# Performance work log

Measured on AMD Instinct MI355X. Metric: run time of the kernel, lower is better.

The kernel has to match this reference:

```python
import jax, jax.numpy as jnp
import numpy as np

B, L, D, H = 4, 2048, 1024, 16
DK = D // H  # 64


def setup_inputs() -> dict:
    key = jax.random.key(0)
    ks = jax.random.split(key, 5)
    x = jax.random.normal(ks[0], (B, L, D), dtype=jnp.float32)
    scale = 1.0 / np.sqrt(D)
    W_qkv = jax.random.normal(ks[1], (D, 3 * D), dtype=jnp.float32) * scale
    b_qkv = jnp.zeros((3 * D,), dtype=jnp.float32)
    W_out = jax.random.normal(ks[2], (D, D), dtype=jnp.float32) * scale
    b_out = jnp.zeros((D,), dtype=jnp.float32)
    return {"x": x, "W_qkv": W_qkv, "b_qkv": b_qkv, "W_out": W_out, "b_out": b_out}


def reference(x, W_qkv, b_qkv, W_out, b_out):
    Bx, Lx, Dx = x.shape
    qkv = x @ W_qkv + b_qkv                      # [B, L, 3D]
    q, k, v = jnp.split(qkv, 3, axis=-1)
    # [B, H, L, d_k]
    q = q.reshape(Bx, Lx, H, DK).transpose(0, 2, 1, 3)
    k = k.reshape(Bx, Lx, H, DK).transpose(0, 2, 1, 3)
    v = v.reshape(Bx, Lx, H, DK).transpose(0, 2, 1, 3)
    scores = jnp.einsum('bhqd,bhkd->bhqk', q, k) / np.sqrt(DK)
    causal = jnp.tril(jnp.ones((Lx, Lx), dtype=bool))
    scores = jnp.where(causal[None, None], scores, -jnp.inf)
    attn = jax.nn.softmax(scores, axis=-1)       # [B, H, L, L]
    out = jnp.einsum('bhqk,bhkd->bhqd', attn, v)
    out = out.transpose(0, 2, 1, 3).reshape(Bx, Lx, Dx)
    return out @ W_out + b_out
```

## Files before the change

kernel.cpp:

```cpp
#include <hip/hip_runtime.h>
#include <stdint.h>

#define B_ 4
#define L_ 2048
#define D_ 1024
#define H_ 16
#define DK_ 64

typedef __attribute__((ext_vector_type(8))) short bf16x8;
typedef __attribute__((ext_vector_type(4))) float f32x4;
typedef unsigned short bfu;

#define MFMA(a, b, c) __builtin_amdgcn_mfma_f32_16x16x32_bf16((a), (b), (c), 0, 0, 0)

__device__ __forceinline__ unsigned short f2bf(float f) {
  union { float f; unsigned int u; } v; v.f = f;
  unsigned int u = v.u;
  return (unsigned short)((u + 0x7fffu + ((u >> 16) & 1u)) >> 16);
}

__device__ __forceinline__ void gll16(const void* g, void* l) {
  __builtin_amdgcn_global_load_lds(
      (const __attribute__((address_space(1))) void*)g,
      (__attribute__((address_space(3))) void*)l, 16, 0, 0);
}


__global__ __launch_bounds__(256) void cast_x(const float* __restrict__ in,
                                              bfu* __restrict__ out, int n4) {
  int i = blockIdx.x * 256 + threadIdx.x;
  if (i >= n4) return;
  float4 v = ((const float4*)in)[i];
  ushort4 o;
  o.x = f2bf(v.x); o.y = f2bf(v.y); o.z = f2bf(v.z); o.w = f2bf(v.w);
  ((ushort4*)out)[i] = o;
}

__global__ void transpose_cast(const float* __restrict__ in, bfu* __restrict__ out,
                               int R, int C) {
  __shared__ float tile[32][33];
  int c0 = blockIdx.x * 32, r0 = blockIdx.y * 32;
  int tx = threadIdx.x, ty = threadIdx.y;
#pragma unroll
  for (int i = ty; i < 32; i += 8)
    tile[i][tx] = in[(size_t)(r0 + i) * C + c0 + tx];
  __syncthreads();
#pragma unroll
  for (int i = ty; i < 32; i += 8)
    out[(size_t)(c0 + i) * R + r0 + tx] = f2bf(tile[tx][i]);
}


template <int EPI>
__global__ __launch_bounds__(512, 2) void gemm8(
    const bfu* __restrict__ A, const bfu* __restrict__ Bt,
    const float* __restrict__ bias, bfu* __restrict__ Qg, bfu* __restrict__ Kg,
    bfu* __restrict__ Vtg, float* __restrict__ Out, int M, int N, int K) {
  __shared__ __align__(16) bfu LDSb[65536];
  const int tid = threadIdx.x;
  const int lane = tid & 63;
  const int w = tid >> 6;
  const int wm = w >> 2, wn = w & 3;
  const int l15 = lane & 15, l4 = lane >> 4;

  const int nwg = gridDim.x;
  const int cpx = nwg >> 3;
  const int bid = (int)blockIdx.x;
  const int swz = (bid & 7) * cpx + (bid >> 3);
  const int m0 = (swz & 31) * 256;
  const int n0 = (swz >> 5) * 256;

#define STAGE(t_, ev_)                                                        \
  {                                                                           \
    const int c_ = (t_) & 1;                                                  \
    bfu* lb_ = ((ev_) == 0 || (ev_) == 3) ? (LDSb + c_ * 16384)               \
                                          : (LDSb + 32768 + c_ * 16384);      \
    const bfu* gs_ = ((ev_) == 0 || (ev_) == 3) ? A : Bt;                     \
    const int g0_ = ((ev_) == 0 || (ev_) == 3) ? m0 : n0;                     \
    _Pragma("unroll") for (int j_ = 0; j_ < 2; ++j_) {                        \
      int idx_ = j_ * 512 + tid;                                              \
      int r7_ = idx_ >> 3;                                                    \
      int row_;                                                               \
      if ((ev_) == 0) row_ = r7_ + ((r7_ >> 6) << 6);                         \
      else if ((ev_) == 3) row_ = 64 + r7_ + ((r7_ >> 6) << 6);               \
      else if ((ev_) == 1) row_ = r7_ + ((r7_ >> 5) << 5);                    \
      else row_ = 32 + r7_ + ((r7_ >> 5) << 5);                               \
      int c16_ = (idx_ & 7) ^ (row_ & 7);                                     \
      gll16(gs_ + (size_t)(g0_ + row_) * K + (t_) * 64 + c16_ * 8,            \
            (char*)lb_ + row_ * 128 + (idx_ & 7) * 16);                       \
    }                                                                         \
  }

#define VMCNT(n_) asm volatile("s_waitcnt vmcnt(" #n_ ")" ::: "memory")
#define BARRIER() asm volatile("s_barrier" ::: "memory")

  f32x4 acc[8][4] = {};
  bf16x8 af[4][2], bfA[2][2], bfB[2][2];

  auto lda = [&](int c, int half) {
    const char* base = (const char*)(LDSb + c * 16384);
#pragma unroll
    for (int mi = 0; mi < 4; ++mi)
#pragma unroll
      for (int kk = 0; kk < 2; ++kk) {
        int row = wm * 128 + half * 64 + mi * 16 + l15;
        int ch = (kk * 4 + l4) ^ (row & 7);
        af[mi][kk] = *(const bf16x8*)(base + row * 128 + ch * 16);
      }
  };
  auto ldb = [&](int c, int half, bf16x8 (*dst)[2]) {
    const char* base = (const char*)(LDSb + 32768 + c * 16384);
#pragma unroll
    for (int ni = 0; ni < 2; ++ni)
#pragma unroll
      for (int kk = 0; kk < 2; ++kk) {
        int row = wn * 64 + half * 32 + ni * 16 + l15;
        int ch = (kk * 4 + l4) ^ (row & 7);
        dst[ni][kk] = *(const bf16x8*)(base + row * 128 + ch * 16);
      }
  };

#define MM(mo_, no_, bfX_)                                                    \
  __builtin_amdgcn_s_setprio(1);                                              \
  _Pragma("unroll") for (int mi_ = 0; mi_ < 4; ++mi_)                         \
  _Pragma("unroll") for (int ni_ = 0; ni_ < 2; ++ni_)                         \
  _Pragma("unroll") for (int kk_ = 0; kk_ < 2; ++kk_)                         \
    acc[(mo_) + mi_][(no_) + ni_] =                                           \
        MFMA(af[mi_][kk_], bfX_[ni_][kk_], acc[(mo_) + mi_][(no_) + ni_]);    \
  __builtin_amdgcn_s_setprio(0);

  STAGE(0, 0); STAGE(0, 1); STAGE(0, 2); STAGE(0, 3);
  VMCNT(4);
  BARRIER();

  const int NT = K >> 6;
  for (int t = 0; t < NT - 1; ++t) {
    const int c = t & 1, tn = t + 1;
    lda(c, 0); ldb(c, 0, bfA);
    STAGE(tn, 0);
    MM(0, 0, bfA);
    VMCNT(4); BARRIER();
    ldb(c, 1, bfB);
    STAGE(tn, 1);
    MM(0, 2, bfB);
    VMCNT(4); BARRIER();
    lda(c, 1);
    STAGE(tn, 2);
    MM(4, 2, bfB);
    BARRIER();
    STAGE(tn, 3);
    MM(4, 0, bfA);
    VMCNT(4); BARRIER();
  }
  {
    const int c = (NT - 1) & 1;
    lda(c, 0); ldb(c, 0, bfA);
    MM(0, 0, bfA);
    VMCNT(2); BARRIER();
    ldb(c, 1, bfB);
    MM(0, 2, bfB);
    VMCNT(0); BARRIER();
    lda(c, 1);
    MM(4, 2, bfB);
    MM(4, 0, bfA);
  }

  if (EPI == 1) {
#pragma unroll
    for (int ni = 0; ni < 4; ++ni) {
      int gn = n0 + wn * 64 + ni * 16 + l15;
      float bv = bias[gn];
#pragma unroll
      for (int mi = 0; mi < 8; ++mi)
#pragma unroll
        for (int rg = 0; rg < 4; ++rg) {
          int gm = m0 + wm * 128 + mi * 16 + l4 * 4 + rg;
          Out[(size_t)gm * N + gn] = acc[mi][ni][rg] + bv;
        }
    }
  } else {
    const int sec = n0 >> 10;
    if (sec < 2) {
      bfu* dst = (sec == 0) ? Qg : Kg;
      const float scale = (sec == 0) ? 0.18033688011112042f : 1.0f;
#pragma unroll
      for (int ni = 0; ni < 4; ++ni) {
        int gn = n0 + wn * 64 + ni * 16 + l15;
        int rem = gn & 1023;
        int hh = rem >> 6, dk = rem & 63;
        float bv = bias[gn];
#pragma unroll
        for (int mi = 0; mi < 8; ++mi)
#pragma unroll
          for (int rg = 0; rg < 4; ++rg) {
            int gm = m0 + wm * 128 + mi * 16 + l4 * 4 + rg;
            int bb = gm >> 11, ll = gm & 2047;
            dst[(((size_t)(bb * H_ + hh)) * L_ + ll) * DK_ + dk] =
                f2bf((acc[mi][ni][rg] + bv) * scale);
          }
      }
    } else {
      __syncthreads();
#pragma unroll
      for (int ni = 0; ni < 4; ++ni) {
        int n_local = wn * 64 + ni * 16 + l15;
        int gn = n0 + n_local;
        float bv = bias[gn];
        int swzn = (n_local & 7) << 4;
#pragma unroll
        for (int mi = 0; mi < 8; ++mi) {
          int m_base = wm * 128 + mi * 16 + l4 * 4;
          int k6 = m_base & 63;
          int p0 = (m_base & ~63) |
                   ((k6 & 32) | (((k6 >> 2) & 3) << 3) | (((k6 >> 4) & 1) << 2));
          float v0 = acc[mi][ni][0] + bv, v1 = acc[mi][ni][1] + bv;
          float v2 = acc[mi][ni][2] + bv, v3 = acc[mi][ni][3] + bv;
          uint32_t w01, w23;
          asm("v_cvt_pk_bf16_f32 %0, %1, %2" : "=v"(w01) : "v"(v0), "v"(v1));
          asm("v_cvt_pk_bf16_f32 %0, %1, %2" : "=v"(w23) : "v"(v2), "v"(v3));
          *(uint32_t*)((char*)LDSb + n_local * 512 + ((2 * p0) ^ swzn)) = w01;
          *(uint32_t*)((char*)LDSb + n_local * 512 + ((2 * p0 + 4) ^ swzn)) = w23;
        }
      }
      __syncthreads();
      int n = tid >> 1;
      int cb = (tid & 1) * 16;
      int gnn = n0 + n;
      int hh = (gnn >> 6) & 15, dk = gnn & 63;
      size_t rowbase =
          (((size_t)((m0 >> 11) * H_ + hh)) * DK_ + dk) * L_ + (m0 & 2047);
#pragma unroll
      for (int j = 0; j < 16; ++j) {
        int ch = cb + j;
        bf16x8 vv = *(const bf16x8*)((char*)LDSb + n * 512 +
                                     ((ch * 16) ^ ((n & 7) << 4)));
        *(bf16x8*)(Vtg + rowbase + ch * 8) = vv;
      }
    }
  }
#undef STAGE
#undef VMCNT
#undef BARRIER
#undef MM
}


__global__ __launch_bounds__(256, 4) void attn(const bfu* __restrict__ Qg,
                                               const bfu* __restrict__ Kg,
                                               const bfu* __restrict__ Vtg,
                                               bfu* __restrict__ Ao) {
  __shared__ __align__(16) bfu Ks[2 * 64 * 64];
  __shared__ __align__(16) bfu Vs[2 * 64 * 64];
  __shared__ __align__(16) bfu Qs[64 * 64];

  const int tid = threadIdx.x;
  const int lane = tid & 63;
  const int w = tid >> 6;
  const int l15 = lane & 15, l4 = lane >> 4;

  const int hid = blockIdx.x;
  const int xcd = hid & 7, slot = hid >> 3;
  const int bh = (xcd << 3) | (slot >> 4);
  const int xq = slot & 15;
  const int b = bh >> 4, h = bh & 15;

  for (int seg = 0; seg < 2; ++seg) {
    const int qb = (seg == 0) ? xq : 31 - xq;
    const int q0 = qb * 64;
    const int nt = qb + 1;

#pragma unroll
    for (int i = 0; i < 2; ++i) {
      int lb = i * 256 + tid;
      int r = lb >> 3, c16 = (lb & 7) ^ (r & 7);
      gll16(Qg + ((size_t)bh * L_ + q0 + r) * DK_ + c16 * 8, (char*)Qs + lb * 16);
      gll16(Kg + ((size_t)bh * L_ + r) * DK_ + c16 * 8, (char*)Ks + lb * 16);
      gll16(Vtg + ((size_t)bh * DK_ + r) * L_ + c16 * 8, (char*)Vs + lb * 16);
    }
    asm volatile("s_waitcnt vmcnt(0)" ::: "memory");
    asm volatile("s_barrier" ::: "memory");

    bf16x8 qf[2];
#pragma unroll
    for (int kk = 0; kk < 2; ++kk) {
      int r = w * 16 + l15;
      int c16 = (kk * 4 + l4) ^ (r & 7);
      qf[kk] = *(const bf16x8*)((const char*)Qs + r * 128 + c16 * 16);
    }

    f32x4 acco[4] = {};
    float m = -1e30f, l = 0.f;

    for (int t = 0; t < nt; ++t) {
      const int cur = t & 1;
      const char* Kc = (const char*)Ks + cur * 8192;
      const char* Vc = (const char*)Vs + cur * 8192;

      if (t + 1 < nt) {
        const int nb = (t + 1) & 1, nkv = (t + 1) * 64;
#pragma unroll
        for (int i = 0; i < 2; ++i) {
          int lb = i * 256 + tid;
          int r = lb >> 3, c16 = (lb & 7) ^ (r & 7);
          gll16(Kg + ((size_t)bh * L_ + nkv + r) * DK_ + c16 * 8,
                (char*)Ks + nb * 8192 + lb * 16);
          gll16(Vtg + ((size_t)bh * DK_ + r) * L_ + nkv + c16 * 8,
                (char*)Vs + nb * 8192 + lb * 16);
        }
        asm volatile("s_waitcnt vmcnt(4)" ::: "memory");
      } else {
        asm volatile("s_waitcnt vmcnt(0)" ::: "memory");
      }
      asm volatile("s_barrier" ::: "memory");

      f32x4 s[4] = {};
      __builtin_amdgcn_s_setprio(1);
#pragma unroll
      for (int kk = 0; kk < 2; ++kk)
#pragma unroll
        for (int ni = 0; ni < 4; ++ni) {
          int r = ni * 16 + l15;
          int c16 = (kk * 4 + l4) ^ (r & 7);
          bf16x8 kf = *(const bf16x8*)(Kc + r * 128 + c16 * 16);
          s[ni] = MFMA(kf, qf[kk], s[ni]);
        }
      __builtin_amdgcn_s_setprio(0);

      if (t == nt - 1) {
        int ql = w * 16 + l15;
#pragma unroll
        for (int ni = 0; ni < 4; ++ni) {
          int kvl = ni * 16 + l4 * 4;
#pragma unroll
          for (int rg = 0; rg < 4; ++rg)
            if (kvl + rg > ql) s[ni][rg] = -1e30f;
        }
      }

      float mx = fmaxf(fmaxf(fmaxf(s[0][0], s[0][1]), fmaxf(s[0][2], s[0][3])),
                       fmaxf(fmaxf(s[1][0], s[1][1]), fmaxf(s[1][2], s[1][3])));
      mx = fmaxf(mx, fmaxf(fmaxf(fmaxf(s[2][0], s[2][1]), fmaxf(s[2][2], s[2][3])),
                           fmaxf(fmaxf(s[3][0], s[3][1]), fmaxf(s[3][2], s[3][3]))));
      mx = fmaxf(mx, __shfl_xor(mx, 16));
      mx = fmaxf(mx, __shfl_xor(mx, 32));
      if (__any(mx - m > 11.0f)) {
        float mn = fmaxf(m, mx);
        float sc = __builtin_amdgcn_exp2f(m - mn);
        m = mn;
        l *= sc;
#pragma unroll
        for (int rg = 0; rg < 4; ++rg) {
          float scq = __shfl(sc, l4 * 4 + rg);
          acco[0][rg] *= scq; acco[1][rg] *= scq;
          acco[2][rg] *= scq; acco[3][rg] *= scq;
        }
      }

      uint32_t pk[4][2];
#pragma unroll
      for (int ni = 0; ni < 4; ++ni) {
        float p0 = __builtin_amdgcn_exp2f(s[ni][0] - m);
        float p1 = __builtin_amdgcn_exp2f(s[ni][1] - m);
        float p2 = __builtin_amdgcn_exp2f(s[ni][2] - m);
        float p3 = __builtin_amdgcn_exp2f(s[ni][3] - m);
        l += (p0 + p1) + (p2 + p3);
        asm("v_cvt_pk_bf16_f32 %0, %1, %2" : "=v"(pk[ni][0]) : "v"(p0), "v"(p1));
        asm("v_cvt_pk_bf16_f32 %0, %1, %2" : "=v"(pk[ni][1]) : "v"(p2), "v"(p3));
      }

      __builtin_amdgcn_s_setprio(1);
#pragma unroll
      for (int kk = 0; kk < 2; ++kk) {
        union { uint32_t wd[4]; bf16x8 v; } u;
        u.wd[0] = pk[2 * kk][0];
        u.wd[1] = pk[2 * kk][1];
        u.wd[2] = pk[2 * kk + 1][0];
        u.wd[3] = pk[2 * kk + 1][1];
#pragma unroll
        for (int ni = 0; ni < 4; ++ni) {
          int r = ni * 16 + l15;
          int c16 = (kk * 4 + l4) ^ (r & 7);
          bf16x8 vf = *(const bf16x8*)(Vc + r * 128 + c16 * 16);
          acco[ni] = MFMA(u.v, vf, acco[ni]);
        }
      }
      __builtin_amdgcn_s_setprio(0);

      asm volatile("s_barrier" ::: "memory");
    }

    float ls = l;
    ls += __shfl_xor(ls, 16);
    ls += __shfl_xor(ls, 32);
    float linv = 1.0f / ls;
#pragma unroll
    for (int rg = 0; rg < 4; ++rg) {
      float lq = __shfl(linv, l4 * 4 + rg);
      int q = q0 + w * 16 + l4 * 4 + rg;
#pragma unroll
      for (int ni = 0; ni < 4; ++ni) {
        int d = ni * 16 + l15;
        Ao[((size_t)b * L_ + q) * D_ + h * DK_ + d] = f2bf(acco[ni][rg] * lq);
      }
    }
  }
}


extern "C" void kernel_launch(void* const* d_in, const int* in_sizes, int n_in,
                              void* d_out, int out_size, void* d_ws, size_t ws_size,
                              hipStream_t stream) {
  const float* x = (const float*)d_in[0];
  const float* W_qkv = (const float*)d_in[1];
  const float* b_qkv = (const float*)d_in[2];
  const float* W_out = (const float*)d_in[3];
  const float* b_out = (const float*)d_in[4];
  float* out = (float*)d_out;

  char* ws = (char*)d_ws;
  bfu* xb     = (bfu*)(ws);
  bfu* Wqkv_t = (bfu*)(ws + 16777216);
  bfu* Wout_t = (bfu*)(ws + 23068672);
  bfu* Qg     = (bfu*)(ws + 25165824);
  bfu* Kg     = (bfu*)(ws + 41943040);
  bfu* Vtg    = (bfu*)(ws + 58720256);
  bfu* Ao     = (bfu*)(ws + 75497472);

  cast_x<<<8192, 256, 0, stream>>>(x, xb, 2097152);
  transpose_cast<<<dim3(96, 32), dim3(32, 8), 0, stream>>>(W_qkv, Wqkv_t, 1024, 3072);
  transpose_cast<<<dim3(32, 32), dim3(32, 8), 0, stream>>>(W_out, Wout_t, 1024, 1024);

  gemm8<0><<<384, 512, 0, stream>>>(xb, Wqkv_t, b_qkv, Qg, Kg, Vtg, nullptr,
                                    8192, 3072, 1024);
  attn<<<1024, 256, 0, stream>>>(Qg, Kg, Vtg, Ao);
  gemm8<1><<<128, 512, 0, stream>>>(Ao, Wout_t, b_out, nullptr, nullptr, nullptr,
                                    out, 8192, 1024, 1024);
}
```

Before: 181.7 us.

## Enlarge attention Q tile to 128 rows, load Q to registers, add GEMM barriers

The attention kernel now gives each block a 128-row Q tile, with 32 rows per wave, and halves the grid. Every K/V tile staged in LDS is therefore reused across twice as many queries. Q fragments are read straight from global memory into registers, which drops the Q LDS buffer, and per-wave causal skipping and masking handle the diagonal. Occupancy is lowered to 3 blocks per CU to allow more registers. The GEMM main loop also gains extra barriers between the staging loads and the MFMA blocks, which adds synchronisation that may cost time.

```diff
diff --git a/kernel.cpp b/kernel.cpp
--- a/kernel.cpp
+++ b/kernel.cpp
@@ -24,6 +24,9 @@
       (const __attribute__((address_space(1))) void*)g,
       (__attribute__((address_space(3))) void*)l, 16, 0, 0);
 }
+
+#define VMCNT(n_) asm volatile("s_waitcnt vmcnt(" #n_ ")" ::: "memory")
+#define BARRIER() asm volatile("s_barrier" ::: "memory")
 
 
 __global__ __launch_bounds__(256) void cast_x(const float* __restrict__ in,
@@ -91,11 +94,8 @@
     }                                                                         \
   }
 
-#define VMCNT(n_) asm volatile("s_waitcnt vmcnt(" #n_ ")" ::: "memory")
-#define BARRIER() asm volatile("s_barrier" ::: "memory")
-
   f32x4 acc[8][4] = {};
-  bf16x8 af[4][2], bfA[2][2], bfB[2][2];
+  bf16x8 af[4][2], bfLO[2][2], bfHI[2][2];
 
   auto lda = [&](int c, int half) {
     const char* base = (const char*)(LDSb + c * 16384);
@@ -136,33 +136,37 @@
   const int NT = K >> 6;
   for (int t = 0; t < NT - 1; ++t) {
     const int c = t & 1, tn = t + 1;
-    lda(c, 0); ldb(c, 0, bfA);
+    lda(c, 0); ldb(c, 0, bfLO);
     STAGE(tn, 0);
-    MM(0, 0, bfA);
+    BARRIER();
+    MM(0, 0, bfLO);
     VMCNT(4); BARRIER();
-    ldb(c, 1, bfB);
+    ldb(c, 1, bfHI);
     STAGE(tn, 1);
-    MM(0, 2, bfB);
+    BARRIER();
+    MM(0, 2, bfHI);
     VMCNT(4); BARRIER();
     lda(c, 1);
     STAGE(tn, 2);
-    MM(4, 2, bfB);
+    BARRIER();
+    MM(4, 2, bfHI);
     BARRIER();
     STAGE(tn, 3);
-    MM(4, 0, bfA);
+    BARRIER();
+    MM(4, 0, bfLO);
     VMCNT(4); BARRIER();
   }
   {
     const int c = (NT - 1) & 1;
-    lda(c, 0); ldb(c, 0, bfA);
-    MM(0, 0, bfA);
+    lda(c, 0); ldb(c, 0, bfLO);
+    MM(0, 0, bfLO);
     VMCNT(2); BARRIER();
-    ldb(c, 1, bfB);
-    MM(0, 2, bfB);
+    ldb(c, 1, bfHI);
+    MM(0, 2, bfHI);
     VMCNT(0); BARRIER();
     lda(c, 1);
-    MM(4, 2, bfB);
-    MM(4, 0, bfA);
+    MM(4, 2, bfHI);
+    MM(4, 0, bfLO);
   }
 
   if (EPI == 1) {
@@ -239,19 +243,16 @@
     }
   }
 #undef STAGE
-#undef VMCNT
-#undef BARRIER
 #undef MM
 }
 
 
-__global__ __launch_bounds__(256, 4) void attn(const bfu* __restrict__ Qg,
+__global__ __launch_bounds__(256, 3) void attn(const bfu* __restrict__ Qg,
                                                const bfu* __restrict__ Kg,
                                                const bfu* __restrict__ Vtg,
                                                bfu* __restrict__ Ao) {
   __shared__ __align__(16) bfu Ks[2 * 64 * 64];
   __shared__ __align__(16) bfu Vs[2 * 64 * 64];
-  __shared__ __align__(16) bfu Qs[64 * 64];
 
   const int tid = threadIdx.x;
   const int lane = tid & 63;
@@ -260,39 +261,41 @@
 
   const int hid = blockIdx.x;
   const int xcd = hid & 7, slot = hid >> 3;
-  const int bh = (xcd << 3) | (slot >> 4);
-  const int xq = slot & 15;
+  const int bh = xcd * 8 + (slot >> 3);
+  const int p = slot & 7;
   const int b = bh >> 4, h = bh & 15;
 
   for (int seg = 0; seg < 2; ++seg) {
-    const int qb = (seg == 0) ? xq : 31 - xq;
-    const int q0 = qb * 64;
-    const int nt = qb + 1;
+    const int qb = (seg == 0) ? p : 15 - p;
+    const int q0 = qb * 128;
+    const int nt = 2 * qb + 2;
+    const int q0w = q0 + w * 32;
+
+    bf16x8 qf[2][2];
+#pragma unroll
+    for (int mi = 0; mi < 2; ++mi)
+#pragma unroll
+      for (int kk = 0; kk < 2; ++kk)
+        qf[mi][kk] = *(const bf16x8*)(
+            Qg + ((size_t)bh * L_ + q0w + mi * 16 + l15) * DK_ + kk * 32 + l4 * 8);
 
 #pragma unroll
     for (int i = 0; i < 2; ++i) {
       int lb = i * 256 + tid;
       int r = lb >> 3, c16 = (lb & 7) ^ (r & 7);
-      gll16(Qg + ((size_t)bh * L_ + q0 + r) * DK_ + c16 * 8, (char*)Qs + lb * 16);
       gll16(Kg + ((size_t)bh * L_ + r) * DK_ + c16 * 8, (char*)Ks + lb * 16);
       gll16(Vtg + ((size_t)bh * DK_ + r) * L_ + c16 * 8, (char*)Vs + lb * 16);
     }
-    asm volatile("s_waitcnt vmcnt(0)" ::: "memory");
-    asm volatile("s_barrier" ::: "memory");
-
-    bf16x8 qf[2];
-#pragma unroll
-    for (int kk = 0; kk < 2; ++kk) {
-      int r = w * 16 + l15;
-      int c16 = (kk * 4 + l4) ^ (r & 7);
-      qf[kk] = *(const bf16x8*)((const char*)Qs + r * 128 + c16 * 16);
-    }
-
-    f32x4 acco[4] = {};
-    float m = -1e30f, l = 0.f;
+    VMCNT(0);
+    BARRIER();
+
+    f32x4 acco[2][4] = {};
+    float m[2] = {-1e30f, -1e30f};
+    float l[2] = {0.f, 0.f};
 
     for (int t = 0; t < nt; ++t) {
       const int cur = t & 1;
+      const int kv0 = t * 64;
       const char* Kc = (const char*)Ks + cur * 8192;
       const char* Vc = (const char*)Vs + cur * 8192;
 
@@ -307,100 +310,130 @@
           gll16(Vtg + ((size_t)bh * DK_ + r) * L_ + nkv + c16 * 8,
                 (char*)Vs + nb * 8192 + lb * 16);
         }
-        asm volatile("s_waitcnt vmcnt(4)" ::: "memory");
+        VMCNT(4);
       } else {
-        asm volatile("s_waitcnt vmcnt(0)" ::: "memory");
-      }
-      asm volatile("s_barrier" ::: "memory");
-
-      f32x4 s[4] = {};
-      __builtin_amdgcn_s_setprio(1);
-#pragma unroll
-      for (int kk = 0; kk < 2; ++kk)
+        VMCNT(0);
+      }
+      BARRIER();
+
+      if (kv0 <= q0w + 31) {
+        f32x4 s[2][4] = {};
+        __builtin_amdgcn_s_setprio(1);
+#pragma unroll
+        for (int kk = 0; kk < 2; ++kk)
+#pragma unroll
+          for (int ni = 0; ni < 4; ++ni) {
+            int r = ni * 16 + l15;
+            int ch = (kk * 4 + l4) ^ (r & 7);
+            bf16x8 kf = *(const bf16x8*)(Kc + r * 128 + ch * 16);
+#pragma unroll
+            for (int mi = 0; mi < 2; ++mi)
+              s[mi][ni] = MFMA(kf, qf[mi][kk], s[mi][ni]);
+          }
+        __builtin_amdgcn_s_setprio(0);
+
+        if (kv0 + 63 > q0w) {
+#pragma unroll
+          for (int mi = 0; mi < 2; ++mi) {
+            int qg_ = q0w + mi * 16 + l15;
+#pragma unroll
+            for (int ni = 0; ni < 4; ++ni) {
+              int kvg = kv0 + ni * 16 + l4 * 4;
+#pragma unroll
+              for (int rg = 0; rg < 4; ++rg)
+                if (kvg + rg > qg_) s[mi][ni][rg] = -1e30f;
+            }
+          }
+        }
+
+        float mx[2];
+#pragma unroll
+        for (int mi = 0; mi < 2; ++mi) {
+          float v = fmaxf(fmaxf(fmaxf(s[mi][0][0], s[mi][0][1]),
+                                fmaxf(s[mi][0][2], s[mi][0][3])),
+                          fmaxf(fmaxf(s[mi][1][0], s[mi][1][1]),
+                                fmaxf(s[mi][1][2], s[mi][1][3])));
+          v = fmaxf(v, fmaxf(fmaxf(fmaxf(s[mi][2][0], s[mi][2][1]),
+                                   fmaxf(s[mi][2][2], s[mi][2][3])),
+                             fmaxf(fmaxf(s[mi][3][0], s[mi][3][1]),
+                                   fmaxf(s[mi][3][2], s[mi][3][3]))));
+          v = fmaxf(v, __shfl_xor(v, 16));
+          v = fmaxf(v, __shfl_xor(v, 32));
+          mx[mi] = v;
+        }
+        float grow = fmaxf(mx[0] - m[0], mx[1] - m[1]);
+        if (__any(grow > 11.0f)) {
+#pragma unroll
+          for (int mi = 0; mi < 2; ++mi) {
+            float mn = fmaxf(m[mi], mx[mi]);
+            float sc = __builtin_amdgcn_exp2f(m[mi] - mn);
+            m[mi] = mn;
+            l[mi] *= sc;
+#pragma unroll
+            for (int rg = 0; rg < 4; ++rg) {
+              float scq = __shfl(sc, l4 * 4 + rg);
+              acco[mi][0][rg] *= scq; acco[mi][1][rg] *= scq;
+              acco[mi][2][rg] *= scq; acco[mi][3][rg] *= scq;
+            }
+          }
+        }
+
+        uint32_t pk[2][4][2];
+#pragma unroll
+        for (int mi = 0; mi < 2; ++mi)
+#pragma unroll
+          for (int ni = 0; ni < 4; ++ni) {
+            float p0 = __builtin_amdgcn_exp2f(s[mi][ni][0] - m[mi]);
+            float p1 = __builtin_amdgcn_exp2f(s[mi][ni][1] - m[mi]);
+            float p2 = __builtin_amdgcn_exp2f(s[mi][ni][2] - m[mi]);
+            float p3 = __builtin_amdgcn_exp2f(s[mi][ni][3] - m[mi]);
+            l[mi] += (p0 + p1) + (p2 + p3);
+            asm("v_cvt_pk_bf16_f32 %0, %1, %2" : "=v"(pk[mi][ni][0]) : "v"(p0), "v"(p1));
+            asm("v_cvt_pk_bf16_f32 %0, %1, %2" : "=v"(pk[mi][ni][1]) : "v"(p2), "v"(p3));
+          }
+
+        __builtin_amdgcn_s_setprio(1);
+#pragma unroll
+        for (int kk = 0; kk < 2; ++kk) {
+          union { uint32_t wd[4]; bf16x8 v; } u[2];
+#pragma unroll
+          for (int mi = 0; mi < 2; ++mi) {
+            u[mi].wd[0] = pk[mi][2 * kk][0];
+            u[mi].wd[1] = pk[mi][2 * kk][1];
+            u[mi].wd[2] = pk[mi][2 * kk + 1][0];
+            u[mi].wd[3] = pk[mi][2 * kk + 1][1];
+          }
+#pragma unroll
+          for (int ni = 0; ni < 4; ++ni) {
+            int r = ni * 16 + l15;
+            int ch = (kk * 4 + l4) ^ (r & 7);
+            bf16x8 vf = *(const bf16x8*)(Vc + r * 128 + ch * 16);
+#pragma unroll
+            for (int mi = 0; mi < 2; ++mi)
+              acco[mi][ni] = MFMA(u[mi].v, vf, acco[mi][ni]);
+          }
+        }
+        __builtin_amdgcn_s_setprio(0);
+      }
+
+      BARRIER();
+    }
+
+#pragma unroll
+    for (int mi = 0; mi < 2; ++mi) {
+      float ls = l[mi];
+      ls += __shfl_xor(ls, 16);
+      ls += __shfl_xor(ls, 32);
+      float linv = 1.0f / ls;
+#pragma unroll
+      for (int rg = 0; rg < 4; ++rg) {
+        float lq = __shfl(linv, l4 * 4 + rg);
+        int q = q0w + mi * 16 + l4 * 4 + rg;
 #pragma unroll
         for (int ni = 0; ni < 4; ++ni) {
-          int r = ni * 16 + l15;
-          int c16 = (kk * 4 + l4) ^ (r & 7);
-          bf16x8 kf = *(const bf16x8*)(Kc + r * 128 + c16 * 16);
-          s[ni] = MFMA(kf, qf[kk], s[ni]);
-        }
-      __builtin_amdgcn_s_setprio(0);
-
-      if (t == nt - 1) {
-        int ql = w * 16 + l15;
-#pragma unroll
-        for (int ni = 0; ni < 4; ++ni) {
-          int kvl = ni * 16 + l4 * 4;
-#pragma unroll
-          for (int rg = 0; rg < 4; ++rg)
-            if (kvl + rg > ql) s[ni][rg] = -1e30f;
-        }
-      }
-
-      float mx = fmaxf(fmaxf(fmaxf(s[0][0], s[0][1]), fmaxf(s[0][2], s[0][3])),
-                       fmaxf(fmaxf(s[1][0], s[1][1]), fmaxf(s[1][2], s[1][3])));
-      mx = fmaxf(mx, fmaxf(fmaxf(fmaxf(s[2][0], s[2][1]), fmaxf(s[2][2], s[2][3])),
-                           fmaxf(fmaxf(s[3][0], s[3][1]), fmaxf(s[3][2], s[3][3]))));
-      mx = fmaxf(mx, __shfl_xor(mx, 16));
-      mx = fmaxf(mx, __shfl_xor(mx, 32));
-      if (__any(mx - m > 11.0f)) {
-        float mn = fmaxf(m, mx);
-        float sc = __builtin_amdgcn_exp2f(m - mn);
-        m = mn;
-        l *= sc;
-#pragma unroll
-        for (int rg = 0; rg < 4; ++rg) {
-          float scq = __shfl(sc, l4 * 4 + rg);
-          acco[0][rg] *= scq; acco[1][rg] *= scq;
-          acco[2][rg] *= scq; acco[3][rg] *= scq;
-        }
-      }
-
-      uint32_t pk[4][2];
-#pragma unroll
-      for (int ni = 0; ni < 4; ++ni) {
-        float p0 = __builtin_amdgcn_exp2f(s[ni][0] - m);
-        float p1 = __builtin_amdgcn_exp2f(s[ni][1] - m);
-        float p2 = __builtin_amdgcn_exp2f(s[ni][2] - m);
-        float p3 = __builtin_amdgcn_exp2f(s[ni][3] - m);
-        l += (p0 + p1) + (p2 + p3);
-        asm("v_cvt_pk_bf16_f32 %0, %1, %2" : "=v"(pk[ni][0]) : "v"(p0), "v"(p1));
-        asm("v_cvt_pk_bf16_f32 %0, %1, %2" : "=v"(pk[ni][1]) : "v"(p2), "v"(p3));
-      }
-
-      __builtin_amdgcn_s_setprio(1);
-#pragma unroll
-      for (int kk = 0; kk < 2; ++kk) {
-        union { uint32_t wd[4]; bf16x8 v; } u;
-        u.wd[0] = pk[2 * kk][0];
-        u.wd[1] = pk[2 * kk][1];
-        u.wd[2] = pk[2 * kk + 1][0];
-        u.wd[3] = pk[2 * kk + 1][1];
-#pragma unroll
-        for (int ni = 0; ni < 4; ++ni) {
-          int r = ni * 16 + l15;
-          int c16 = (kk * 4 + l4) ^ (r & 7);
-          bf16x8 vf = *(const bf16x8*)(Vc + r * 128 + c16 * 16);
-          acco[ni] = MFMA(u.v, vf, acco[ni]);
-        }
-      }
-      __builtin_amdgcn_s_setprio(0);
-
-      asm volatile("s_barrier" ::: "memory");
-    }
-
-    float ls = l;
-    ls += __shfl_xor(ls, 16);
-    ls += __shfl_xor(ls, 32);
-    float linv = 1.0f / ls;
-#pragma unroll
-    for (int rg = 0; rg < 4; ++rg) {
-      float lq = __shfl(linv, l4 * 4 + rg);
-      int q = q0 + w * 16 + l4 * 4 + rg;
-#pragma unroll
-      for (int ni = 0; ni < 4; ++ni) {
-        int d = ni * 16 + l15;
-        Ao[((size_t)b * L_ + q) * D_ + h * DK_ + d] = f2bf(acco[ni][rg] * lq);
+          int d = ni * 16 + l15;
+          Ao[((size_t)b * L_ + q) * D_ + h * DK_ + d] = f2bf(acco[mi][ni][rg] * lq);
+        }
       }
     }
   }
@@ -432,7 +465,7 @@
 
   gemm8<0><<<384, 512, 0, stream>>>(xb, Wqkv_t, b_qkv, Qg, Kg, Vtg, nullptr,
                                     8192, 3072, 1024);
-  attn<<<1024, 256, 0, stream>>>(Qg, Kg, Vtg, Ao);
+  attn<<<512, 256, 0, stream>>>(Qg, Kg, Vtg, Ao);
   gemm8<1><<<128, 512, 0, stream>>>(Ao, Wout_t, b_out, nullptr, nullptr, nullptr,
                                     out, 8192, 1024, 1024);
 }
```

Result: slower. 185.7 us (+2.2%).
